# Kernel tuning notes

Measured on AMD Instinct MI355X. Metric: run time of the kernel, lower is better.

## Reference

```python
import jax, jax.numpy as jnp
import numpy as np

N_NODES = 50000
N_EDGES = 800000
DIM = 128
N_LAYERS = 5


def setup_inputs() -> dict:
    key = jax.random.key(0)
    k1, k2, k3, k4 = jax.random.split(key, 4)
    x = jax.random.normal(k1, (N_NODES, DIM), dtype=jnp.float32)
    edge_index = jax.random.randint(k2, (2, N_EDGES), 0, N_NODES, dtype=jnp.int64)
    # He-ish scale for stacked GCN layers so activations stay sane
    weights = jax.random.normal(k3, (N_LAYERS, DIM, DIM), dtype=jnp.float32) / jnp.sqrt(jnp.float32(DIM))
    biases = jax.random.normal(k4, (N_LAYERS, DIM), dtype=jnp.float32) * 0.01
    return {"x": x, "edge_index": edge_index, "weights": weights, "biases": biases}


def reference(x, edge_index, weights, biases):
    """5x (GCNConv -> ReLU). GCNConv: out = D^-1/2 (A+I) D^-1/2 (x W) + b."""
    n = x.shape[0]
    src, dst = edge_index[0], edge_index[1]
    # add self-loops (PyG GCNConv default)
    loop = jnp.arange(n, dtype=src.dtype)
    src_f = jnp.concatenate([src, loop])
    dst_f = jnp.concatenate([dst, loop])
    # symmetric normalization based on in-degree (incl. self loops)
    deg = jax.ops.segment_sum(jnp.ones(src_f.shape[0], dtype=x.dtype), dst_f, num_segments=n)
    dinv = jnp.where(deg > 0, jax.lax.rsqrt(deg), 0.0)
    norm = dinv[src_f] * dinv[dst_f]  # [E+N]

    for l in range(weights.shape[0]):
        h = x @ weights[l]                      # [N, D] dense transform
        msg = h[src_f] * norm[:, None]          # gather + scale  [E+N, D]
        x = jax.ops.segment_sum(msg, dst_f, num_segments=n) + biases[l]
        x = jax.nn.relu(x)
    return x
```

## Files before the change

### kernel.cpp

```cpp
#include <hip/hip_runtime.h>
#include <hip/hip_bf16.h>
#include <hip/hip_fp16.h>


#define GCN_DIM 128

typedef short bf16x8 __attribute__((ext_vector_type(8)));
typedef float f32x4 __attribute__((ext_vector_type(4)));

__device__ __forceinline__ unsigned short f2bf(float f) {
    unsigned int u = __float_as_uint(f);
    u += 0x7FFFu + ((u >> 16) & 1u);
    return (unsigned short)(u >> 16);
}
__device__ __forceinline__ float bf2f(unsigned short b) {
    return __uint_as_float(((unsigned int)b) << 16);
}
__device__ __forceinline__ float bflo(unsigned int p) { return __uint_as_float(p << 16); }
__device__ __forceinline__ float bfhi(unsigned int p) { return __uint_as_float(p & 0xFFFF0000u); }

__global__ void count_kernel(const int* __restrict__ dst, int* __restrict__ cnt,
                             int* __restrict__ rank, int E) {
    int e = blockIdx.x * 256 + threadIdx.x;
    if (e < E) rank[e] = atomicAdd(&cnt[dst[e]], 1);
}

__global__ __launch_bounds__(256) void scan_part_kernel(const int* __restrict__ cnt,
                                                        int* __restrict__ loc,
                                                        int* __restrict__ bsum, int n) {
    __shared__ int s[256];
    int t = threadIdx.x;
    int i0 = blockIdx.x * 1024 + t * 4;
    int v0 = (i0 + 0 < n) ? cnt[i0 + 0] : 0;
    int v1 = (i0 + 1 < n) ? cnt[i0 + 1] : 0;
    int v2 = (i0 + 2 < n) ? cnt[i0 + 2] : 0;
    int v3 = (i0 + 3 < n) ? cnt[i0 + 3] : 0;
    int tsum = v0 + v1 + v2 + v3;
    s[t] = tsum;
    __syncthreads();
    for (int d = 1; d < 256; d <<= 1) {
        int u = (t >= d) ? s[t - d] : 0;
        __syncthreads();
        s[t] += u;
        __syncthreads();
    }
    int base = s[t] - tsum;
    if (i0 + 0 < n) loc[i0 + 0] = base; base += v0;
    if (i0 + 1 < n) loc[i0 + 1] = base; base += v1;
    if (i0 + 2 < n) loc[i0 + 2] = base; base += v2;
    if (i0 + 3 < n) loc[i0 + 3] = base;
    if (t == 255) bsum[blockIdx.x] = s[255];
}

__global__ __launch_bounds__(256) void scan_top_kernel(int* __restrict__ bsum, int nb) {
    __shared__ int s[256];
    int t = threadIdx.x;
    int v = (t < nb) ? bsum[t] : 0;
    s[t] = v;
    __syncthreads();
    for (int d = 1; d < 256; d <<= 1) {
        int u = (t >= d) ? s[t - d] : 0;
        __syncthreads();
        s[t] += u;
        __syncthreads();
    }
    if (t < nb) bsum[t] = s[t] - v;
}

__global__ void scan_add_kernel(int* __restrict__ offs,
                                const int* __restrict__ bsum, const int* __restrict__ cnt,
                                float* __restrict__ dinv, int n, int E) {
    int i = blockIdx.x * 256 + threadIdx.x;
    if (i < n) {
        offs[i] = offs[i] + bsum[i >> 10];
        dinv[i] = rsqrtf((float)cnt[i] + 1.0f);
    }
    if (i == 0) offs[n] = E;
}

__global__ void fill_kernel(const int* __restrict__ src, const int* __restrict__ dst,
                            const float* __restrict__ dinv, const int* __restrict__ rank,
                            const int* __restrict__ offs,
                            unsigned int* __restrict__ edat, int E) {
    int e = blockIdx.x * 256 + threadIdx.x;
    if (e < E) {
        int d = dst[e];
        int s = src[e];
        int p = offs[d] + rank[e];
        unsigned short wb = __half_as_ushort(__float2half(dinv[s]));
        edat[p] = (unsigned int)s | ((unsigned int)wb << 16);
    }
}

__global__ void split_x_kernel(const float* __restrict__ x, unsigned short* __restrict__ xh,
                               unsigned short* __restrict__ xl, int total) {
    int i = (blockIdx.x * 256 + threadIdx.x) * 4;
    if (i >= total) return;
    float4 v = *(const float4*)&x[i];
    ushort4 h4, l4;
    h4.x = f2bf(v.x); l4.x = f2bf(v.x - bf2f(h4.x));
    h4.y = f2bf(v.y); l4.y = f2bf(v.y - bf2f(h4.y));
    h4.z = f2bf(v.z); l4.z = f2bf(v.z - bf2f(h4.z));
    h4.w = f2bf(v.w); l4.w = f2bf(v.w - bf2f(h4.w));
    *(ushort4*)&xh[i] = h4;
    *(ushort4*)&xl[i] = l4;
}

__global__ void wsplit_kernel(const float* __restrict__ Wall, unsigned short* __restrict__ Wfh,
                              unsigned short* __restrict__ Wfl, int total) {
    int idx = blockIdx.x * 256 + threadIdx.x;
    if (idx >= total) return;
    int l = idx >> 14;
    int rem = idx & 16383;
    int k = rem >> 7;
    int nn = rem & 127;
    float v = Wall[idx];
    unsigned short hi = f2bf(v);
    unsigned short lo = f2bf(v - bf2f(hi));
    int t = nn >> 4, ln = nn & 15;
    int ks = k >> 5, q = (k >> 3) & 3, j = k & 7;
    int o = ((((l << 5) | (t << 2) | ks) << 6) | (q << 4) | ln) * 8 + j;
    Wfh[o] = hi;
    Wfl[o] = lo;
}

__global__ __launch_bounds__(256) void gemm_mfma_kernel(
    const unsigned short* __restrict__ xh, const unsigned short* __restrict__ xl,
    const unsigned short* __restrict__ Wfh, const unsigned short* __restrict__ Wfl,
    unsigned short* __restrict__ h, int n) {
    __shared__ unsigned short ldsW[2][8192];
    int tid = threadIdx.x;
    int wave = tid >> 6, lane = tid & 63;
    int q = lane >> 4, ln = lane & 15;
    int rowbase = blockIdx.x * 64 + wave * 16;
    bf16x8 A[4][2];
    {
        int ar = rowbase + ln;
        if (ar >= n) ar = n - 1;
        size_t base = (size_t)ar * GCN_DIM;
#pragma unroll
        for (int ks = 0; ks < 4; ks++) {
            A[ks][0] = *(const bf16x8*)&xh[base + ks * 32 + q * 8];
            A[ks][1] = *(const bf16x8*)&xl[base + ks * 32 + q * 8];
        }
    }
    int node = rowbase + ln;
#pragma unroll
    for (int half = 0; half < 2; half++) {
        if (half) __syncthreads();
        {
            const uint4* gh = (const uint4*)(Wfh + half * 8192);
            const uint4* gl = (const uint4*)(Wfl + half * 8192);
            uint4* sh = (uint4*)ldsW[0];
            uint4* sl = (uint4*)ldsW[1];
#pragma unroll
            for (int r = 0; r < 4; r++) {
                sh[tid + 256 * r] = gh[tid + 256 * r];
                sl[tid + 256 * r] = gl[tid + 256 * r];
            }
        }
        __syncthreads();
#pragma unroll
        for (int tp = 0; tp < 2; tp++) {
            int tta = tp * 2, ttb = tp * 2 + 1;
            f32x4 accA = (f32x4)(0.f), accB = (f32x4)(0.f);
#pragma unroll
            for (int ks = 0; ks < 4; ks++) {
                int foA = ((tta * 4 + ks) * 64 + lane) * 8;
                int foB = ((ttb * 4 + ks) * 64 + lane) * 8;
                bf16x8 bhA = *(const bf16x8*)&ldsW[0][foA];
                bf16x8 blA = *(const bf16x8*)&ldsW[1][foA];
                bf16x8 bhB = *(const bf16x8*)&ldsW[0][foB];
                bf16x8 blB = *(const bf16x8*)&ldsW[1][foB];
                accA = __builtin_amdgcn_mfma_f32_16x16x32_bf16(bhA, A[ks][0], accA, 0, 0, 0);
                accB = __builtin_amdgcn_mfma_f32_16x16x32_bf16(bhB, A[ks][0], accB, 0, 0, 0);
                accA = __builtin_amdgcn_mfma_f32_16x16x32_bf16(bhA, A[ks][1], accA, 0, 0, 0);
                accB = __builtin_amdgcn_mfma_f32_16x16x32_bf16(bhB, A[ks][1], accB, 0, 0, 0);
                accA = __builtin_amdgcn_mfma_f32_16x16x32_bf16(blA, A[ks][0], accA, 0, 0, 0);
                accB = __builtin_amdgcn_mfma_f32_16x16x32_bf16(blB, A[ks][0], accB, 0, 0, 0);
            }
            if (node < n) {
                int ta = half * 4 + tta, tb = half * 4 + ttb;
                ushort4 oA, oB;
                oA.x = f2bf(accA[0]); oA.y = f2bf(accA[1]);
                oA.z = f2bf(accA[2]); oA.w = f2bf(accA[3]);
                oB.x = f2bf(accB[0]); oB.y = f2bf(accB[1]);
                oB.z = f2bf(accB[2]); oB.w = f2bf(accB[3]);
                *(ushort4*)&h[((size_t)ta * n + node) * 16 + q * 4] = oA;
                *(ushort4*)&h[((size_t)tb * n + node) * 16 + q * 4] = oB;
            }
        }
    }
}

__global__ __launch_bounds__(256) void agg_kernel(
    const unsigned short* __restrict__ h,
    const unsigned int* __restrict__ edat,
    const int* __restrict__ offs,
    const float* __restrict__ dinv, const float* __restrict__ bias,
    unsigned short* __restrict__ xh_out,
    unsigned short* __restrict__ xl_out,
    float* __restrict__ fout, int n) {
    int tid = threadIdx.x;
    int wave = tid >> 6, lane = tid & 63;
    int sub = lane >> 3, ln = lane & 7;
    int slice = blockIdx.x & 7;
    int node = (blockIdx.x >> 3) * 32 + wave * 8 + sub;
    if (node >= n) return;
    size_t sbase = (size_t)slice * n;
    int fo = ln * 2;
    float di = dinv[node];
    unsigned int sp = *(const unsigned int*)&h[(sbase + node) * 16 + fo];
    float ax0 = di * bflo(sp), ay0 = di * bfhi(sp);
    float ax1 = 0.f, ay1 = 0.f, ax2 = 0.f, ay2 = 0.f, ax3 = 0.f, ay3 = 0.f;
    int s = offs[node], e = offs[node + 1];
    int j = s;
    for (; j + 8 <= e; j += 8) {
        unsigned int v0 = edat[j], v1 = edat[j + 1], v2 = edat[j + 2], v3 = edat[j + 3];
        unsigned int v4 = edat[j + 4], v5 = edat[j + 5], v6 = edat[j + 6], v7 = edat[j + 7];
        unsigned int p0 = *(const unsigned int*)&h[(sbase + (v0 & 0xFFFFu)) * 16 + fo];
        unsigned int p1 = *(const unsigned int*)&h[(sbase + (v1 & 0xFFFFu)) * 16 + fo];
        unsigned int p2 = *(const unsigned int*)&h[(sbase + (v2 & 0xFFFFu)) * 16 + fo];
        unsigned int p3 = *(const unsigned int*)&h[(sbase + (v3 & 0xFFFFu)) * 16 + fo];
        unsigned int p4 = *(const unsigned int*)&h[(sbase + (v4 & 0xFFFFu)) * 16 + fo];
        unsigned int p5 = *(const unsigned int*)&h[(sbase + (v5 & 0xFFFFu)) * 16 + fo];
        unsigned int p6 = *(const unsigned int*)&h[(sbase + (v6 & 0xFFFFu)) * 16 + fo];
        unsigned int p7 = *(const unsigned int*)&h[(sbase + (v7 & 0xFFFFu)) * 16 + fo];
        float w0 = __half2float(__ushort_as_half((unsigned short)(v0 >> 16)));
        float w1 = __half2float(__ushort_as_half((unsigned short)(v1 >> 16)));
        float w2 = __half2float(__ushort_as_half((unsigned short)(v2 >> 16)));
        float w3 = __half2float(__ushort_as_half((unsigned short)(v3 >> 16)));
        float w4 = __half2float(__ushort_as_half((unsigned short)(v4 >> 16)));
        float w5 = __half2float(__ushort_as_half((unsigned short)(v5 >> 16)));
        float w6 = __half2float(__ushort_as_half((unsigned short)(v6 >> 16)));
        float w7 = __half2float(__ushort_as_half((unsigned short)(v7 >> 16)));
        ax0 = fmaf(w0, bflo(p0), ax0); ay0 = fmaf(w0, bfhi(p0), ay0);
        ax1 = fmaf(w1, bflo(p1), ax1); ay1 = fmaf(w1, bfhi(p1), ay1);
        ax2 = fmaf(w2, bflo(p2), ax2); ay2 = fmaf(w2, bfhi(p2), ay2);
        ax3 = fmaf(w3, bflo(p3), ax3); ay3 = fmaf(w3, bfhi(p3), ay3);
        ax0 = fmaf(w4, bflo(p4), ax0); ay0 = fmaf(w4, bfhi(p4), ay0);
        ax1 = fmaf(w5, bflo(p5), ax1); ay1 = fmaf(w5, bfhi(p5), ay1);
        ax2 = fmaf(w6, bflo(p6), ax2); ay2 = fmaf(w6, bfhi(p6), ay2);
        ax3 = fmaf(w7, bflo(p7), ax3); ay3 = fmaf(w7, bfhi(p7), ay3);
    }
    for (; j + 4 <= e; j += 4) {
        unsigned int v0 = edat[j], v1 = edat[j + 1], v2 = edat[j + 2], v3 = edat[j + 3];
        unsigned int p0 = *(const unsigned int*)&h[(sbase + (v0 & 0xFFFFu)) * 16 + fo];
        unsigned int p1 = *(const unsigned int*)&h[(sbase + (v1 & 0xFFFFu)) * 16 + fo];
        unsigned int p2 = *(const unsigned int*)&h[(sbase + (v2 & 0xFFFFu)) * 16 + fo];
        unsigned int p3 = *(const unsigned int*)&h[(sbase + (v3 & 0xFFFFu)) * 16 + fo];
        float w0 = __half2float(__ushort_as_half((unsigned short)(v0 >> 16)));
        float w1 = __half2float(__ushort_as_half((unsigned short)(v1 >> 16)));
        float w2 = __half2float(__ushort_as_half((unsigned short)(v2 >> 16)));
        float w3 = __half2float(__ushort_as_half((unsigned short)(v3 >> 16)));
        ax0 = fmaf(w0, bflo(p0), ax0); ay0 = fmaf(w0, bfhi(p0), ay0);
        ax1 = fmaf(w1, bflo(p1), ax1); ay1 = fmaf(w1, bfhi(p1), ay1);
        ax2 = fmaf(w2, bflo(p2), ax2); ay2 = fmaf(w2, bfhi(p2), ay2);
        ax3 = fmaf(w3, bflo(p3), ax3); ay3 = fmaf(w3, bfhi(p3), ay3);
    }
    for (; j < e; j++) {
        unsigned int v0 = edat[j];
        unsigned int p0 = *(const unsigned int*)&h[(sbase + (v0 & 0xFFFFu)) * 16 + fo];
        float w0 = __half2float(__ushort_as_half((unsigned short)(v0 >> 16)));
        ax0 = fmaf(w0, bflo(p0), ax0);
        ay0 = fmaf(w0, bfhi(p0), ay0);
    }
    float ax = (ax0 + ax1) + (ax2 + ax3);
    float ay = (ay0 + ay1) + (ay2 + ay3);
    int cg = slice * 16 + fo;
    float2 b = *(const float2*)&bias[cg];
    float rx = fmaxf(fmaf(di, ax, b.x), 0.f);
    float ry = fmaxf(fmaf(di, ay, b.y), 0.f);
    if (fout) {
        unsigned long long pv = (unsigned long long)__float_as_uint(rx) |
                                ((unsigned long long)__float_as_uint(ry) << 32);
        __builtin_nontemporal_store(pv, (unsigned long long*)&fout[(size_t)node * GCN_DIM + cg]);
    } else {
        unsigned short hx = f2bf(rx), hy = f2bf(ry);
        unsigned int hp = (unsigned int)hx | ((unsigned int)hy << 16);
        unsigned short lx = f2bf(rx - bf2f(hx)), ly = f2bf(ry - bf2f(hy));
        unsigned int lp = (unsigned int)lx | ((unsigned int)ly << 16);
        __builtin_nontemporal_store(hp, (unsigned int*)&xh_out[(size_t)node * GCN_DIM + cg]);
        __builtin_nontemporal_store(lp, (unsigned int*)&xl_out[(size_t)node * GCN_DIM + cg]);
    }
}

extern "C" void kernel_launch(void* const* d_in, const int* in_sizes, int n_in,
                              void* d_out, int out_size, void* d_ws, size_t ws_size,
                              hipStream_t stream) {
    const float* x0    = (const float*)d_in[0];
    const int*   edges = (const int*)d_in[1];
    const float* Wall  = (const float*)d_in[2];
    const float* Ball  = (const float*)d_in[3];
    float* out = (float*)d_out;

    const int n = in_sizes[0] / GCN_DIM;
    const int E = in_sizes[1] / 2;
    const int L = in_sizes[2] / (GCN_DIM * GCN_DIM);

    int*   cnt    = (int*)d_ws;
    float* dinv   = (float*)(cnt + n);
    int*   offs   = (int*)(dinv + n);
    int*   bsum   = offs + n + 16;
    int*   rank   = bsum + 64;
    unsigned int* edat = (unsigned int*)(rank + E);
    unsigned short* h   = (unsigned short*)(edat + E);
    unsigned short* xh  = h  + (size_t)n * GCN_DIM;
    unsigned short* xl  = xh + (size_t)n * GCN_DIM;
    unsigned short* Wfh = xl + (size_t)n * GCN_DIM;
    unsigned short* Wfl = Wfh + (size_t)L * GCN_DIM * GCN_DIM;

    const int* src = edges;
    const int* dst = edges + E;

    int nb_n = (n + 255) / 256;
    int nb_e = (E + 255) / 256;
    int nb_scan = (n + 1023) / 1024;

    hipMemsetAsync(cnt, 0, (size_t)n * sizeof(int), stream);
    count_kernel<<<nb_e, 256, 0, stream>>>(dst, cnt, rank, E);
    scan_part_kernel<<<nb_scan, 256, 0, stream>>>(cnt, offs, bsum, n);
    scan_top_kernel<<<1, 256, 0, stream>>>(bsum, nb_scan);
    scan_add_kernel<<<nb_n, 256, 0, stream>>>(offs, bsum, cnt, dinv, n, E);
    fill_kernel<<<nb_e, 256, 0, stream>>>(src, dst, dinv, rank, offs, edat, E);

    int xtotal = n * GCN_DIM;
    split_x_kernel<<<(xtotal / 4 + 255) / 256, 256, 0, stream>>>(x0, xh, xl, xtotal);
    int wtotal = L * GCN_DIM * GCN_DIM;
    wsplit_kernel<<<(wtotal + 255) / 256, 256, 0, stream>>>(Wall, Wfh, Wfl, wtotal);

    int gemm_blocks = (n + 63) / 64;
    int agg_blocks  = ((n + 31) / 32) * 8;

    for (int l = 0; l < L; l++) {
        gemm_mfma_kernel<<<gemm_blocks, 256, 0, stream>>>(
            xh, xl, Wfh + (size_t)l * GCN_DIM * GCN_DIM, Wfl + (size_t)l * GCN_DIM * GCN_DIM, h, n);
        agg_kernel<<<agg_blocks, 256, 0, stream>>>(
            h, edat, offs, dinv, Ball + (size_t)l * GCN_DIM,
            xh, xl, (l == L - 1) ? out : nullptr, n);
    }
}
```

Baseline: 409.7 us.

## Fold source-degree scaling into GEMM epilogue and store byte offsets in edge list

Multiplies the GEMM output rows by dinv of the source node before storing, so the aggregation kernel no longer needs a per-edge fp16 weight and can do plain adds. The edge entries now hold pre-shifted byte offsets (src<<5), which removes the masking and index arithmetic from the gather address computation. This cuts ALU work per edge in the gather-bound aggregation and drops the fp16 weight rounding. The h values are now rounded to bf16 after scaling, which slightly changes numerics.

```diff
diff --git a/kernel.cpp b/kernel.cpp
--- a/kernel.cpp
+++ b/kernel.cpp
@@ -79,16 +79,13 @@
 }
 
 __global__ void fill_kernel(const int* __restrict__ src, const int* __restrict__ dst,
-                            const float* __restrict__ dinv, const int* __restrict__ rank,
-                            const int* __restrict__ offs,
+                            const int* __restrict__ rank, const int* __restrict__ offs,
                             unsigned int* __restrict__ edat, int E) {
     int e = blockIdx.x * 256 + threadIdx.x;
     if (e < E) {
         int d = dst[e];
-        int s = src[e];
         int p = offs[d] + rank[e];
-        unsigned short wb = __half_as_ushort(__float2half(dinv[s]));
-        edat[p] = (unsigned int)s | ((unsigned int)wb << 16);
+        edat[p] = ((unsigned int)src[e]) << 5;
     }
 }
 
@@ -127,6 +124,7 @@
 __global__ __launch_bounds__(256) void gemm_mfma_kernel(
     const unsigned short* __restrict__ xh, const unsigned short* __restrict__ xl,
     const unsigned short* __restrict__ Wfh, const unsigned short* __restrict__ Wfl,
+    const float* __restrict__ dinv,
     unsigned short* __restrict__ h, int n) {
     __shared__ unsigned short ldsW[2][8192];
     int tid = threadIdx.x;
@@ -145,6 +143,7 @@
         }
     }
     int node = rowbase + ln;
+    float di = (node < n) ? dinv[node] : 0.f;
 #pragma unroll
     for (int half = 0; half < 2; half++) {
         if (half) __syncthreads();
@@ -182,10 +181,10 @@
             if (node < n) {
                 int ta = half * 4 + tta, tb = half * 4 + ttb;
                 ushort4 oA, oB;
-                oA.x = f2bf(accA[0]); oA.y = f2bf(accA[1]);
-                oA.z = f2bf(accA[2]); oA.w = f2bf(accA[3]);
-                oB.x = f2bf(accB[0]); oB.y = f2bf(accB[1]);
-                oB.z = f2bf(accB[2]); oB.w = f2bf(accB[3]);
+                oA.x = f2bf(accA[0] * di); oA.y = f2bf(accA[1] * di);
+                oA.z = f2bf(accA[2] * di); oA.w = f2bf(accA[3] * di);
+                oB.x = f2bf(accB[0] * di); oB.y = f2bf(accB[1] * di);
+                oB.z = f2bf(accB[2] * di); oB.w = f2bf(accB[3] * di);
                 *(ushort4*)&h[((size_t)ta * n + node) * 16 + q * 4] = oA;
                 *(ushort4*)&h[((size_t)tb * n + node) * 16 + q * 4] = oB;
             }
@@ -207,67 +206,57 @@
     int slice = blockIdx.x & 7;
     int node = (blockIdx.x >> 3) * 32 + wave * 8 + sub;
     if (node >= n) return;
-    size_t sbase = (size_t)slice * n;
-    int fo = ln * 2;
+    const char* hs = (const char*)h + (size_t)slice * n * 32;
+    unsigned int fo2 = (unsigned int)(ln << 2);
     float di = dinv[node];
-    unsigned int sp = *(const unsigned int*)&h[(sbase + node) * 16 + fo];
-    float ax0 = di * bflo(sp), ay0 = di * bfhi(sp);
+    unsigned int sp = *(const unsigned int*)(hs + (unsigned int)node * 32u + fo2);
+    float ax0 = bflo(sp), ay0 = bfhi(sp);
     float ax1 = 0.f, ay1 = 0.f, ax2 = 0.f, ay2 = 0.f, ax3 = 0.f, ay3 = 0.f;
     int s = offs[node], e = offs[node + 1];
     int j = s;
     for (; j + 8 <= e; j += 8) {
-        unsigned int v0 = edat[j], v1 = edat[j + 1], v2 = edat[j + 2], v3 = edat[j + 3];
-        unsigned int v4 = edat[j + 4], v5 = edat[j + 5], v6 = edat[j + 6], v7 = edat[j + 7];
-        unsigned int p0 = *(const unsigned int*)&h[(sbase + (v0 & 0xFFFFu)) * 16 + fo];
-        unsigned int p1 = *(const unsigned int*)&h[(sbase + (v1 & 0xFFFFu)) * 16 + fo];
-        unsigned int p2 = *(const unsigned int*)&h[(sbase + (v2 & 0xFFFFu)) * 16 + fo];
-        unsigned int p3 = *(const unsigned int*)&h[(sbase + (v3 & 0xFFFFu)) * 16 + fo];
-        unsigned int p4 = *(const unsigned int*)&h[(sbase + (v4 & 0xFFFFu)) * 16 + fo];
-        unsigned int p5 = *(const unsigned int*)&h[(sbase + (v5 & 0xFFFFu)) * 16 + fo];
-        unsigned int p6 = *(const unsigned int*)&h[(sbase + (v6 & 0xFFFFu)) * 16 + fo];
-        unsigned int p7 = *(const unsigned int*)&h[(sbase + (v7 & 0xFFFFu)) * 16 + fo];
-        float w0 = __half2float(__ushort_as_half((unsigned short)(v0 >> 16)));
-        float w1 = __half2float(__ushort_as_half((unsigned short)(v1 >> 16)));
-        float w2 = __half2float(__ushort_as_half((unsigned short)(v2 >> 16)));
-        float w3 = __half2float(__ushort_as_half((unsigned short)(v3 >> 16)));
-        float w4 = __half2float(__ushort_as_half((unsigned short)(v4 >> 16)));
-        float w5 = __half2float(__ushort_as_half((unsigned short)(v5 >> 16)));
-        float w6 = __half2float(__ushort_as_half((unsigned short)(v6 >> 16)));
-        float w7 = __half2float(__ushort_as_half((unsigned short)(v7 >> 16)));
-        ax0 = fmaf(w0, bflo(p0), ax0); ay0 = fmaf(w0, bfhi(p0), ay0);
-        ax1 = fmaf(w1, bflo(p1), ax1); ay1 = fmaf(w1, bfhi(p1), ay1);
-        ax2 = fmaf(w2, bflo(p2), ax2); ay2 = fmaf(w2, bfhi(p2), ay2);
-        ax3 = fmaf(w3, bflo(p3), ax3); ay3 = fmaf(w3, bfhi(p3), ay3);
-        ax0 = fmaf(w4, bflo(p4), ax0); ay0 = fmaf(w4, bfhi(p4), ay0);
-        ax1 = fmaf(w5, bflo(p5), ax1); ay1 = fmaf(w5, bfhi(p5), ay1);
-        ax2 = fmaf(w6, bflo(p6), ax2); ay2 = fmaf(w6, bfhi(p6), ay2);
-        ax3 = fmaf(w7, bflo(p7), ax3); ay3 = fmaf(w7, bfhi(p7), ay3);
+        unsigned int v0 = edat[j] + fo2, v1 = edat[j + 1] + fo2;
+        unsigned int v2 = edat[j + 2] + fo2, v3 = edat[j + 3] + fo2;
+        unsigned int v4 = edat[j + 4] + fo2, v5 = edat[j + 5] + fo2;
+        unsigned int v6 = edat[j + 6] + fo2, v7 = edat[j + 7] + fo2;
+        unsigned int p0 = *(const unsigned int*)(hs + v0);
+        unsigned int p1 = *(const unsigned int*)(hs + v1);
+        unsigned int p2 = *(const unsigned int*)(hs + v2);
+        unsigned int p3 = *(const unsigned int*)(hs + v3);
+        unsigned int p4 = *(const unsigned int*)(hs + v4);
+        unsigned int p5 = *(const unsigned int*)(hs + v5);
+        unsigned int p6 = *(const unsigned int*)(hs + v6);
+        unsigned int p7 = *(const unsigned int*)(hs + v7);
+        ax0 += bflo(p0); ay0 += bfhi(p0);
+        ax1 += bflo(p1); ay1 += bfhi(p1);
+        ax2 += bflo(p2); ay2 += bfhi(p2);
+        ax3 += bflo(p3); ay3 += bfhi(p3);
+        ax0 += bflo(p4); ay0 += bfhi(p4);
+        ax1 += bflo(p5); ay1 += bfhi(p5);
+        ax2 += bflo(p6); ay2 += bfhi(p6);
+        ax3 += bflo(p7); ay3 += bfhi(p7);
     }
     for (; j + 4 <= e; j += 4) {
-        unsigned int v0 = edat[j], v1 = edat[j + 1], v2 = edat[j + 2], v3 = edat[j + 3];
-        unsigned int p0 = *(const unsigned int*)&h[(sbase + (v0 & 0xFFFFu)) * 16 + fo];
-        unsigned int p1 = *(const unsigned int*)&h[(sbase + (v1 & 0xFFFFu)) * 16 + fo];
-        unsigned int p2 = *(const unsigned int*)&h[(sbase + (v2 & 0xFFFFu)) * 16 + fo];
-        unsigned int p3 = *(const unsigned int*)&h[(sbase + (v3 & 0xFFFFu)) * 16 + fo];
-        float w0 = __half2float(__ushort_as_half((unsigned short)(v0 >> 16)));
-        float w1 = __half2float(__ushort_as_half((unsigned short)(v1 >> 16)));
-        float w2 = __half2float(__ushort_as_half((unsigned short)(v2 >> 16)));
-        float w3 = __half2float(__ushort_as_half((unsigned short)(v3 >> 16)));
-        ax0 = fmaf(w0, bflo(p0), ax0); ay0 = fmaf(w0, bfhi(p0), ay0);
-        ax1 = fmaf(w1, bflo(p1), ax1); ay1 = fmaf(w1, bfhi(p1), ay1);
-        ax2 = fmaf(w2, bflo(p2), ax2); ay2 = fmaf(w2, bfhi(p2), ay2);
-        ax3 = fmaf(w3, bflo(p3), ax3); ay3 = fmaf(w3, bfhi(p3), ay3);
+        unsigned int v0 = edat[j] + fo2, v1 = edat[j + 1] + fo2;
+        unsigned int v2 = edat[j + 2] + fo2, v3 = edat[j + 3] + fo2;
+        unsigned int p0 = *(const unsigned int*)(hs + v0);
+        unsigned int p1 = *(const unsigned int*)(hs + v1);
+        unsigned int p2 = *(const unsigned int*)(hs + v2);
+        unsigned int p3 = *(const unsigned int*)(hs + v3);
+        ax0 += bflo(p0); ay0 += bfhi(p0);
+        ax1 += bflo(p1); ay1 += bfhi(p1);
+        ax2 += bflo(p2); ay2 += bfhi(p2);
+        ax3 += bflo(p3); ay3 += bfhi(p3);
     }
     for (; j < e; j++) {
-        unsigned int v0 = edat[j];
-        unsigned int p0 = *(const unsigned int*)&h[(sbase + (v0 & 0xFFFFu)) * 16 + fo];
-        float w0 = __half2float(__ushort_as_half((unsigned short)(v0 >> 16)));
-        ax0 = fmaf(w0, bflo(p0), ax0);
-        ay0 = fmaf(w0, bfhi(p0), ay0);
+        unsigned int v0 = edat[j] + fo2;
+        unsigned int p0 = *(const unsigned int*)(hs + v0);
+        ax0 += bflo(p0);
+        ay0 += bfhi(p0);
     }
     float ax = (ax0 + ax1) + (ax2 + ax3);
     float ay = (ay0 + ay1) + (ay2 + ay3);
-    int cg = slice * 16 + fo;
+    int cg = slice * 16 + (ln << 1);
     float2 b = *(const float2*)&bias[cg];
     float rx = fmaxf(fmaf(di, ax, b.x), 0.f);
     float ry = fmaxf(fmaf(di, ay, b.y), 0.f);
@@ -322,7 +311,7 @@
     scan_part_kernel<<<nb_scan, 256, 0, stream>>>(cnt, offs, bsum, n);
     scan_top_kernel<<<1, 256, 0, stream>>>(bsum, nb_scan);
     scan_add_kernel<<<nb_n, 256, 0, stream>>>(offs, bsum, cnt, dinv, n, E);
-    fill_kernel<<<nb_e, 256, 0, stream>>>(src, dst, dinv, rank, offs, edat, E);
+    fill_kernel<<<nb_e, 256, 0, stream>>>(src, dst, rank, offs, edat, E);
 
     int xtotal = n * GCN_DIM;
     split_x_kernel<<<(xtotal / 4 + 255) / 256, 256, 0, stream>>>(x0, xh, xl, xtotal);
@@ -334,7 +323,8 @@
 
     for (int l = 0; l < L; l++) {
         gemm_mfma_kernel<<<gemm_blocks, 256, 0, stream>>>(
-            xh, xl, Wfh + (size_t)l * GCN_DIM * GCN_DIM, Wfl + (size_t)l * GCN_DIM * GCN_DIM, h, n);
+            xh, xl, Wfh + (size_t)l * GCN_DIM * GCN_DIM, Wfl + (size_t)l * GCN_DIM * GCN_DIM,
+            dinv, h, n);
         agg_kernel<<<agg_blocks, 256, 0, stream>>>(
             h, edat, offs, dinv, Ball + (size_t)l * GCN_DIM,
             xh, xl, (l == L - 1) ? out : nullptr, n);
```

Result: no change. 407.7 us, median of 2 (-0.5%).
